# Kernel tuning notes

Hardware: AMD Instinct MI355X
Metric: run time of the kernel (lower is better)

Reference implementation:

```python
import jax, jax.numpy as jnp
import numpy as np

K_NB = 20  # num_neighbors

def _gather_nb(vals, idx):
    # vals: (B,N,D), idx: (B,N,K) -> (B,N,K,D)
    return jax.vmap(lambda v, i: v[i])(vals, idx)

def _pt_layer(x, pos, qkv_w, pw1, pb1, pw2, pb2, aw1, ab1, aw2, ab2):
    # x: (B,N,C), pos: (B,N,3)
    qkv = x @ qkv_w                      # (B,N,3C)
    q, k, v = jnp.split(qkv, 3, axis=-1)
    # squared euclidean distances (monotone in cdist -> same knn indices)
    d2 = jnp.sum((pos[:, :, None, :] - pos[:, None, :, :]) ** 2, axis=-1)  # (B,N,N)
    _, idx = jax.lax.top_k(-d2, K_NB)    # (B,N,K) smallest distances (incl. self)
    p2 = _gather_nb(pos, idx)            # (B,N,K,3)
    rel_pos = pos[:, :, None, :] - p2
    rel_pos_emb = jax.nn.relu(rel_pos @ pw1 + pb1) @ pw2 + pb2  # (B,N,K,C)
    k_nb = _gather_nb(k, idx)            # (B,N,K,C)
    qk_rel = q[:, :, None, :] - k_nb
    v_nb = _gather_nb(v, idx) + rel_pos_emb
    inp = jnp.concatenate([qk_rel, rel_pos_emb], axis=-1)  # (B,N,K,2C)
    sim = jax.nn.relu(inp @ aw1 + ab1) @ aw2 + ab2          # (B,N,K,1)
    attn = jax.nn.softmax(sim, axis=-2)
    return jnp.sum(attn * v_nb, axis=2)  # (B,N,C)

def setup_inputs() -> dict:
    key = jax.random.key(0)
    ks = jax.random.split(key, 32)
    B, N = 2, 8192
    s = 0.05
    d = {}
    d['points'] = jax.random.uniform(ks[0], (B, N, 3), jnp.float32)
    d['conv_w'] = jax.random.normal(ks[1], (3, 64), jnp.float32) * s
    d['conv_b'] = jax.random.normal(ks[2], (64,), jnp.float32) * s
    i = 3
    for L in ('l1', 'l2'):
        d[L + '_qkv'] = jax.random.normal(ks[i], (64, 192), jnp.float32) * s; i += 1
        d[L + '_pw1'] = jax.random.normal(ks[i], (3, 64), jnp.float32) * s; i += 1
        d[L + '_pb1'] = jax.random.normal(ks[i], (64,), jnp.float32) * s; i += 1
        d[L + '_pw2'] = jax.random.normal(ks[i], (64, 64), jnp.float32) * s; i += 1
        d[L + '_pb2'] = jax.random.normal(ks[i], (64,), jnp.float32) * s; i += 1
        d[L + '_aw1'] = jax.random.normal(ks[i], (128, 256), jnp.float32) * s; i += 1
        d[L + '_ab1'] = jax.random.normal(ks[i], (256,), jnp.float32) * s; i += 1
        d[L + '_aw2'] = jax.random.normal(ks[i], (256, 1), jnp.float32) * s; i += 1
        d[L + '_ab2'] = jax.random.normal(ks[i], (1,), jnp.float32) * s; i += 1
    d['fc1_w'] = jax.random.normal(ks[i], (64, 32), jnp.float32) * s; i += 1
    d['fc1_b'] = jax.random.normal(ks[i], (32,), jnp.float32) * s; i += 1
    d['fc3_w'] = jax.random.normal(ks[i], (32, 3), jnp.float32) * s; i += 1
    d['fc3_b'] = jax.random.normal(ks[i], (3,), jnp.float32) * s
    return d

def reference(points, conv_w, conv_b,
              l1_qkv, l1_pw1, l1_pb1, l1_pw2, l1_pb2, l1_aw1, l1_ab1, l1_aw2, l1_ab2,
              l2_qkv, l2_pw1, l2_pb1, l2_pw2, l2_pb2, l2_aw1, l2_ab1, l2_aw2, l2_ab2,
              fc1_w, fc1_b, fc3_w, fc3_b):
    pos = points
    out = jax.nn.relu(points @ conv_w + conv_b)  # Conv1d(3,64,1) == pointwise linear
    out = _pt_layer(out, pos, l1_qkv, l1_pw1, l1_pb1, l1_pw2, l1_pb2, l1_aw1, l1_ab1, l1_aw2, l1_ab2)
    out = _pt_layer(out, pos, l2_qkv, l2_pw1, l2_pb1, l2_pw2, l2_pb2, l2_aw1, l2_ab1, l2_aw2, l2_ab2)
    out = jnp.max(out, axis=1)                    # global max-pool over N
    out = jax.nn.relu(out @ fc1_w + fc1_b)
    return out @ fc3_w + fc3_b                    # (B, num_classes)
```

## Files before the change

kernel.cpp:

```cpp
#include <hip/hip_runtime.h>
#include <cstdint>
#include <cstddef>

#define KNB 20
#define NPTS 8192
#define BATCH 2
#define TOTAL (BATCH * NPTS)

__global__ __launch_bounds__(256) void k_conv(const float* __restrict__ pts,
                                              const float* __restrict__ w,
                                              const float* __restrict__ b,
                                              float* __restrict__ x0,
                                              float* __restrict__ ptsT) {
  int gid = blockIdx.x * 256 + threadIdx.x;
  if (gid >= TOTAL * 64) return;
  int p = gid >> 6, c = gid & 63;
  float px = pts[p * 3 + 0], py = pts[p * 3 + 1], pz = pts[p * 3 + 2];
  float acc = b[c] + px * w[c] + py * w[64 + c] + pz * w[128 + c];
  x0[gid] = fmaxf(acc, 0.f);
  if (c < 3) {
    int bb = p >> 13, pp = p & (NPTS - 1);
    ptsT[((size_t)bb * 3 + c) * NPTS + pp] = pts[p * 3 + c];
  }
}

__global__ __launch_bounds__(256) void k_knn(const float* __restrict__ ptsT,
                                             const float* __restrict__ pts,
                                             int* __restrict__ idxbuf) {
  int tid = threadIdx.x;
  int wv = tid >> 6, lane = tid & 63;
  int q = blockIdx.x * 4 + wv;
  int bq = q >> 13;
  const float* px = ptsT + (size_t)bq * 3 * NPTS;
  const float* py = px + NPTS;
  const float* pz = py + NPTS;
  float qx = pts[q * 3 + 0], qy = pts[q * 3 + 1], qz = pts[q * 3 + 2];

  float dist[KNB];
  int id[KNB];
#pragma unroll
  for (int j = 0; j < KNB; j++) { dist[j] = 3.402823466e38f; id[j] = 0; }
  float tau = 3.402823466e38f;

#define INSERT(D2, CID)                                                      \
  if ((D2) <= tau && (D2) < dist[KNB - 1]) {                                 \
    int cid_ = (CID);                                                        \
    _Pragma("unroll")                                                        \
    for (int j = KNB - 1; j >= 0; j--) {                                     \
      bool cj = (D2) < dist[j];                                              \
      bool cjm1 = (j > 0) && ((D2) < dist[j - 1]);                           \
      if (cj) {                                                              \
        dist[j] = cjm1 ? dist[j - 1] : (D2);                                 \
        id[j]   = cjm1 ? id[j - 1]   : cid_;                                 \
      }                                                                      \
    }                                                                        \
  }

  for (int chunk = 0; chunk < 8; chunk++) {
    if (chunk) {
      float h = dist[0];
#pragma unroll
      for (int k = 2; k <= 64; k <<= 1) {
#pragma unroll
        for (int j = k >> 1; j > 0; j >>= 1) {
          float o = __shfl_xor(h, j);
          bool up = ((lane & k) == 0);
          bool lower = ((lane & j) == 0);
          bool takeMin = (up == lower);
          bool lt = h < o;
          h = (takeMin == lt) ? h : o;
        }
      }
      tau = __shfl(h, 19);
    }

    int base = chunk * 1024;
#pragma unroll
    for (int g = 0; g < 4; g++) {
      int cb = base + g * 256 + lane * 4;
      float4 x4 = *(const float4*)&px[cb];
      float4 y4 = *(const float4*)&py[cb];
      float4 z4 = *(const float4*)&pz[cb];
      float dx0 = qx - x4.x, dy0 = qy - y4.x, dz0 = qz - z4.x;
      float dx1 = qx - x4.y, dy1 = qy - y4.y, dz1 = qz - z4.y;
      float dx2 = qx - x4.z, dy2 = qy - y4.z, dz2 = qz - z4.z;
      float dx3 = qx - x4.w, dy3 = qy - y4.w, dz3 = qz - z4.w;
      float d0 = __fadd_rn(__fadd_rn(__fmul_rn(dx0, dx0), __fmul_rn(dy0, dy0)),
                           __fmul_rn(dz0, dz0));
      float d1 = __fadd_rn(__fadd_rn(__fmul_rn(dx1, dx1), __fmul_rn(dy1, dy1)),
                           __fmul_rn(dz1, dz1));
      float d2v = __fadd_rn(__fadd_rn(__fmul_rn(dx2, dx2), __fmul_rn(dy2, dy2)),
                            __fmul_rn(dz2, dz2));
      float d3 = __fadd_rn(__fadd_rn(__fmul_rn(dx3, dx3), __fmul_rn(dy3, dy3)),
                           __fmul_rn(dz3, dz3));
      INSERT(d0, cb + 0)
      INSERT(d1, cb + 1)
      INSERT(d2v, cb + 2)
      INSERT(d3, cb + 3)
    }
  }
#undef INSERT

  int bqoff = bq * NPTS;
  for (int step = 0; step < KNB; step++) {
    unsigned long long p =
        ((unsigned long long)__float_as_uint(dist[0]) << 32) | (unsigned)id[0];
    unsigned long long m = p;
#pragma unroll
    for (int off = 32; off >= 1; off >>= 1) {
      unsigned long long o = __shfl_xor(m, off);
      m = (o < m) ? o : m;
    }
    if (lane == 0) idxbuf[q * KNB + step] = bqoff + (int)(m & 0xffffffffULL);
    if (p == m) {
#pragma unroll
      for (int j = 0; j < KNB - 1; j++) { dist[j] = dist[j + 1]; id[j] = id[j + 1]; }
      dist[KNB - 1] = 3.402823466e38f;
    }
  }
}

__global__ __launch_bounds__(256) void k_w2(const float* __restrict__ pw2,
                                            const float* __restrict__ pb2,
                                            const float* __restrict__ aw1,
                                            float* __restrict__ W2,
                                            float* __restrict__ c0) {
  int h = blockIdx.x, c = threadIdx.x;
  float a = 0.f;
  if (h < 64) {
#pragma unroll 8
    for (int j = 0; j < 64; j++)
      a += pw2[h * 64 + j] * aw1[(size_t)(64 + j) * 256 + c];
    W2[h * 256 + c] = a;
  } else {
#pragma unroll 8
    for (int j = 0; j < 64; j++)
      a += pb2[j] * aw1[(size_t)(64 + j) * 256 + c];
    c0[c] = a;
  }
}

__global__ __launch_bounds__(256) void k_pre(const float* __restrict__ x,
                                             const float* __restrict__ w,
                                             const float* __restrict__ aw1,
                                             const float* __restrict__ c0,
                                             float* __restrict__ v,
                                             float* __restrict__ kh,
                                             float* __restrict__ qh) {
  int tid = threadIdx.x;
  int wv = tid >> 6, lane = tid & 63;
  int p = blockIdx.x * 4 + wv;
  const float* xr = x + (size_t)p * 64;

  float qa = 0.f, ka = 0.f, va = 0.f;
#pragma unroll 8
  for (int h = 0; h < 64; h++) {
    float xv = xr[h];
    qa += xv * w[h * 192 + lane];
    ka += xv * w[h * 192 + 64 + lane];
    va += xv * w[h * 192 + 128 + lane];
  }
  v[(size_t)p * 64 + lane] = va;

#define RL(x_, l_) __uint_as_float(__builtin_amdgcn_readlane(__float_as_uint(x_), (l_)))
  int c4 = lane * 4;
  float4 a = make_float4(0.f, 0.f, 0.f, 0.f);
#pragma unroll 8
  for (int h = 0; h < 64; h++) {
    float kb = RL(ka, h);
    float4 wv4 = *(const float4*)&aw1[(size_t)h * 256 + c4];
    a.x += kb * wv4.x; a.y += kb * wv4.y; a.z += kb * wv4.z; a.w += kb * wv4.w;
  }
  *(float4*)&kh[(size_t)p * 256 + c4] = a;

  float4 b = make_float4(0.f, 0.f, 0.f, 0.f);
#pragma unroll 8
  for (int h = 0; h < 64; h++) {
    float qb = RL(qa, h);
    float4 wv4 = *(const float4*)&aw1[(size_t)h * 256 + c4];
    b.x += qb * wv4.x; b.y += qb * wv4.y; b.z += qb * wv4.z; b.w += qb * wv4.w;
  }
#undef RL
  float4 c04 = *(const float4*)&c0[c4];
  b.x += c04.x; b.y += c04.y; b.z += c04.z; b.w += c04.w;
  *(float4*)&qh[(size_t)p * 256 + c4] = b;
}

__global__ __launch_bounds__(256) void k_attn(
    const float* __restrict__ pos, const float* __restrict__ v,
    const int* __restrict__ idxbuf, const float* __restrict__ kh,
    const float* __restrict__ qh,
    const float* __restrict__ pw1, const float* __restrict__ pb1,
    const float* __restrict__ pw2, const float* __restrict__ pb2,
    const float* __restrict__ W2, const float* __restrict__ ab1,
    const float* __restrict__ aw2, const float* __restrict__ ab2,
    float* __restrict__ xout) {
  __shared__ float s_t1[4][KNB][64];
  __shared__ float s_sim[4][KNB];
  __shared__ int   s_nb[4][24];

  int tid = threadIdx.x;
  int wv = tid >> 6, lane = tid & 63;
  int i = blockIdx.x * 4 + wv;

  if (lane < KNB) s_nb[wv][lane] = idxbuf[i * KNB + lane];
  float px = pos[i * 3 + 0], py = pos[i * 3 + 1], pz = pos[i * 3 + 2];
  __syncthreads();

#define RL(x, l) __uint_as_float(__builtin_amdgcn_readlane(__float_as_uint(x), (l)))
  float t1[KNB];
  float vnb[KNB];
  {
    float w1x = pw1[lane], w1y = pw1[64 + lane], w1z = pw1[128 + lane];
    float b1h = pb1[lane];
#pragma unroll
    for (int n = 0; n < KNB; n++) {
      int g = s_nb[wv][n];
      vnb[n] = v[(size_t)g * 64 + lane];
      float rx = px - pos[g * 3 + 0];
      float ry = py - pos[g * 3 + 1];
      float rz = pz - pos[g * 3 + 2];
      t1[n] = fmaxf(b1h + rx * w1x + ry * w1y + rz * w1z, 0.f);
      s_t1[wv][n][lane] = t1[n];
    }
  }
  __syncthreads();

  int col0 = lane * 4;
  float4 qh4 = *(const float4*)&qh[(size_t)i * 256 + col0];

  float4 b1v = *(const float4*)&ab1[col0];
  float4 w2v = *(const float4*)&aw2[col0];
  float ab2v = ab2[0];
#pragma unroll
  for (int pass = 0; pass < 4; pass++) {
    int nb0 = pass * 5;
    float acc[5][4];
#pragma unroll
    for (int n = 0; n < 5; n++) {
      int g = s_nb[wv][nb0 + n];
      float4 kv = *(const float4*)&kh[(size_t)g * 256 + col0];
      acc[n][0] = qh4.x - kv.x; acc[n][1] = qh4.y - kv.y;
      acc[n][2] = qh4.z - kv.z; acc[n][3] = qh4.w - kv.w;
    }
#pragma unroll 2
    for (int kc = 0; kc < 64; kc += 4) {
      float4 w0 = *(const float4*)&W2[(kc + 0) * 256 + col0];
      float4 w1 = *(const float4*)&W2[(kc + 1) * 256 + col0];
      float4 w2 = *(const float4*)&W2[(kc + 2) * 256 + col0];
      float4 w3 = *(const float4*)&W2[(kc + 3) * 256 + col0];
#pragma unroll
      for (int n = 0; n < 5; n++) {
        float4 iv = *(float4*)&s_t1[wv][nb0 + n][kc];
        acc[n][0] += iv.x * w0.x + iv.y * w1.x + iv.z * w2.x + iv.w * w3.x;
        acc[n][1] += iv.x * w0.y + iv.y * w1.y + iv.z * w2.y + iv.w * w3.y;
        acc[n][2] += iv.x * w0.z + iv.y * w1.z + iv.z * w2.z + iv.w * w3.z;
        acc[n][3] += iv.x * w0.w + iv.y * w1.w + iv.z * w2.w + iv.w * w3.w;
      }
    }
#pragma unroll
    for (int n = 0; n < 5; n++) {
      float s = fmaxf(acc[n][0] + b1v.x, 0.f) * w2v.x +
                fmaxf(acc[n][1] + b1v.y, 0.f) * w2v.y +
                fmaxf(acc[n][2] + b1v.z, 0.f) * w2v.z +
                fmaxf(acc[n][3] + b1v.w, 0.f) * w2v.w;
#pragma unroll
      for (int off = 32; off >= 1; off >>= 1) s += __shfl_xor(s, off);
      if (lane == 0) s_sim[wv][nb0 + n] = s + ab2v;
    }
  }
  __syncthreads();

  float mx = -3.402823466e38f;
#pragma unroll
  for (int n = 0; n < KNB; n++) mx = fmaxf(mx, s_sim[wv][n]);
  float sum = 0.f;
#pragma unroll
  for (int n = 0; n < KNB; n++) sum += expf(s_sim[wv][n] - mx);
  float inv = 1.f / sum;
  float o = 0.f;
  float sac = 0.f;
#pragma unroll
  for (int n = 0; n < KNB; n++) {
    float an = expf(s_sim[wv][n] - mx) * inv;
    o += an * vnb[n];
    sac += an * t1[n];
  }
  float r = pb2[lane];
#pragma unroll 8
  for (int j = 0; j < 64; j++) r += RL(sac, j) * pw2[j * 64 + lane];
#undef RL
  xout[(size_t)i * 64 + lane] = o + r;
}

__global__ __launch_bounds__(256) void k_pool(const float* __restrict__ x,
                                              float* __restrict__ pmax) {
  __shared__ float red[4][64];
  int b = blockIdx.x >> 6, blk = blockIdx.x & 63;
  int tid = threadIdx.x;
  int c = tid & 63, pg = tid >> 6;
  int p0 = blk * 128;
  float mx = -3.402823466e38f;
  for (int p = pg; p < 128; p += 4)
    mx = fmaxf(mx, x[((size_t)b * NPTS + p0 + p) * 64 + c]);
  red[pg][c] = mx;
  __syncthreads();
  if (tid < 64)
    pmax[(size_t)blockIdx.x * 64 + c] =
        fmaxf(fmaxf(red[0][c], red[1][c]), fmaxf(red[2][c], red[3][c]));
}

__global__ __launch_bounds__(256) void k_final2(const float* __restrict__ pmax,
                                                const float* __restrict__ fc1w,
                                                const float* __restrict__ fc1b,
                                                const float* __restrict__ fc3w,
                                                const float* __restrict__ fc3b,
                                                float* __restrict__ out) {
  __shared__ float red[4][64];
  __shared__ float m[64];
  __shared__ float h1[32];
  int b = blockIdx.x;
  int tid = threadIdx.x;
  int c = tid & 63, pg = tid >> 6;
  float mx = -3.402823466e38f;
  for (int blk = pg; blk < 64; blk += 4)
    mx = fmaxf(mx, pmax[(size_t)(b * 64 + blk) * 64 + c]);
  red[pg][c] = mx;
  __syncthreads();
  if (tid < 64)
    m[c] = fmaxf(fmaxf(red[0][c], red[1][c]), fmaxf(red[2][c], red[3][c]));
  __syncthreads();
  if (tid < 32) {
    float a = fc1b[tid];
#pragma unroll 8
    for (int k = 0; k < 64; k++) a += m[k] * fc1w[k * 32 + tid];
    h1[tid] = fmaxf(a, 0.f);
  }
  __syncthreads();
  if (tid < 3) {
    float a = fc3b[tid];
#pragma unroll
    for (int k = 0; k < 32; k++) a += h1[k] * fc3w[k * 3 + tid];
    out[b * 3 + tid] = a;
  }
}

extern "C" void kernel_launch(void* const* d_in, const int* in_sizes, int n_in,
                              void* d_out, int out_size, void* d_ws,
                              size_t ws_size, hipStream_t stream) {
  const float* pts    = (const float*)d_in[0];
  const float* conv_w = (const float*)d_in[1];
  const float* conv_b = (const float*)d_in[2];
  const float* fc1w = (const float*)d_in[21];
  const float* fc1b = (const float*)d_in[22];
  const float* fc3w = (const float*)d_in[23];
  const float* fc3b = (const float*)d_in[24];
  float* outp = (float*)d_out;

  char* ws = (char*)d_ws;
  int*   idx  = (int*)  (ws);
  float* ptsT = (float*)(ws + (size_t)1536 * 1024);
  float* W2   = (float*)(ws + (size_t)1792 * 1024);
  float* c0   = (float*)(ws + (size_t)1862 * 1024);
  float* pmax = (float*)(ws + (size_t)1900 * 1024);
  float* v    = (float*)(ws + (size_t)2 * 1048576);
  float* kh   = (float*)(ws + (size_t)6656 * 1024);
  float* qh   = (float*)(ws + (size_t)24064 * 1024);
  float* act  = (float*)(ws + (size_t)41472 * 1024);

  k_conv<<<(TOTAL * 64 + 255) / 256, 256, 0, stream>>>(pts, conv_w, conv_b,
                                                       act, ptsT);
  k_knn<<<TOTAL / 4, 256, 0, stream>>>(ptsT, pts, idx);

  for (int layer = 0; layer < 2; layer++) {
    int base = 3 + layer * 9;
    const float* qkvw = (const float*)d_in[base + 0];
    const float* pw1  = (const float*)d_in[base + 1];
    const float* pb1  = (const float*)d_in[base + 2];
    const float* pw2  = (const float*)d_in[base + 3];
    const float* pb2  = (const float*)d_in[base + 4];
    const float* aw1  = (const float*)d_in[base + 5];
    const float* ab1  = (const float*)d_in[base + 6];
    const float* aw2  = (const float*)d_in[base + 7];
    const float* ab2  = (const float*)d_in[base + 8];
    k_w2<<<65, 256, 0, stream>>>(pw2, pb2, aw1, W2, c0);
    k_pre<<<TOTAL / 4, 256, 0, stream>>>(act, qkvw, aw1, c0, v, kh, qh);
    k_attn<<<TOTAL / 4, 256, 0, stream>>>(
        pts, v, idx, kh, qh, pw1, pb1, pw2, pb2, W2, ab1, aw2, ab2, act);
  }
  k_pool<<<BATCH * 64, 256, 0, stream>>>(act, pmax);
  k_final2<<<BATCH, 256, 0, stream>>>(pmax, fc1w, fc1b, fc3w, fc3b, outp);
}
```

Baseline: 1.027 ms.

## Replace brute-force kNN with uniform-grid spatial binning and local search

Points are binned into a 16^3 uniform grid per batch using histogram, scan and scatter kernels. Each query then searches only a 7x7x7 cell neighbourhood, and falls back to a full brute-force scan pruned by the 20th-smallest distance when that radius cannot guarantee exactness. This replaces the O(N^2) distance scan with mostly local work, at the cost of four extra small launches and divergent per-lane loops over cell ranges. Keys pack distance and original index into 64 bits so tie-breaking stays by index.

```diff
diff --git a/kernel.cpp b/kernel.cpp
--- a/kernel.cpp
+++ b/kernel.cpp
@@ -6,105 +6,178 @@
 #define NPTS 8192
 #define BATCH 2
 #define TOTAL (BATCH * NPTS)
+#define NCELL 4096
+#define SENT 0x7F800000FFFFFFFFULL
 
 __global__ __launch_bounds__(256) void k_conv(const float* __restrict__ pts,
                                               const float* __restrict__ w,
                                               const float* __restrict__ b,
-                                              float* __restrict__ x0,
-                                              float* __restrict__ ptsT) {
+                                              float* __restrict__ x0) {
   int gid = blockIdx.x * 256 + threadIdx.x;
   if (gid >= TOTAL * 64) return;
   int p = gid >> 6, c = gid & 63;
   float px = pts[p * 3 + 0], py = pts[p * 3 + 1], pz = pts[p * 3 + 2];
   float acc = b[c] + px * w[c] + py * w[64 + c] + pz * w[128 + c];
   x0[gid] = fmaxf(acc, 0.f);
-  if (c < 3) {
-    int bb = p >> 13, pp = p & (NPTS - 1);
-    ptsT[((size_t)bb * 3 + c) * NPTS + pp] = pts[p * 3 + c];
-  }
-}
-
-__global__ __launch_bounds__(256) void k_knn(const float* __restrict__ ptsT,
-                                             const float* __restrict__ pts,
-                                             int* __restrict__ idxbuf) {
+}
+
+__global__ __launch_bounds__(256) void k_zero(int* __restrict__ cnt) {
+  int g = blockIdx.x * 256 + threadIdx.x;
+  if (g < 2 * BATCH * NCELL) cnt[g] = 0;
+}
+
+__global__ __launch_bounds__(256) void k_hist(const float* __restrict__ pts,
+                                              int* __restrict__ cnt) {
+  int p = blockIdx.x * 256 + threadIdx.x;
+  if (p >= TOTAL) return;
+  int b = p >> 13;
+  int cx = min(15, (int)(pts[p * 3 + 0] * 16.f));
+  int cy = min(15, (int)(pts[p * 3 + 1] * 16.f));
+  int cz = min(15, (int)(pts[p * 3 + 2] * 16.f));
+  atomicAdd(&cnt[b * NCELL + (cz * 16 + cy) * 16 + cx], 1);
+}
+
+__global__ __launch_bounds__(256) void k_scan(const int* __restrict__ cnt,
+                                              int* __restrict__ cellStart) {
+  __shared__ int ls[256];
+  int b = blockIdx.x, t = threadIdx.x;
+  const int* c = cnt + b * NCELL;
+  int* cs = cellStart + b * (NCELL + 1);
+  int base = t * 16;
+  int s = 0;
+#pragma unroll
+  for (int i = 0; i < 16; i++) s += c[base + i];
+  ls[t] = s;
+  __syncthreads();
+  for (int off = 1; off < 256; off <<= 1) {
+    int v = (t >= off) ? ls[t - off] : 0;
+    __syncthreads();
+    ls[t] += v;
+    __syncthreads();
+  }
+  int run = ls[t] - s;
+#pragma unroll
+  for (int i = 0; i < 16; i++) { cs[base + i] = run; run += c[base + i]; }
+  if (t == 255) cs[NCELL] = run;
+}
+
+__global__ __launch_bounds__(256) void k_scatter(
+    const float* __restrict__ pts, int* __restrict__ cnt2,
+    const int* __restrict__ cellStart, float* __restrict__ sx,
+    float* __restrict__ sy, float* __restrict__ sz, int* __restrict__ sidx) {
+  int p = blockIdx.x * 256 + threadIdx.x;
+  if (p >= TOTAL) return;
+  int b = p >> 13, pl = p & (NPTS - 1);
+  float x = pts[p * 3 + 0], y = pts[p * 3 + 1], z = pts[p * 3 + 2];
+  int cx = min(15, (int)(x * 16.f));
+  int cy = min(15, (int)(y * 16.f));
+  int cz = min(15, (int)(z * 16.f));
+  int cell = (cz * 16 + cy) * 16 + cx;
+  int pos = cellStart[b * (NCELL + 1) + cell] + atomicAdd(&cnt2[b * NCELL + cell], 1);
+  size_t o = (size_t)b * NPTS + pos;
+  sx[o] = x; sy[o] = y; sz[o] = z; sidx[o] = pl;
+}
+
+__global__ __launch_bounds__(256) void k_knn(
+    const float* __restrict__ pts, const float* __restrict__ sx,
+    const float* __restrict__ sy, const float* __restrict__ sz,
+    const int* __restrict__ sidx, const int* __restrict__ cellStart,
+    int* __restrict__ idxbuf) {
   int tid = threadIdx.x;
   int wv = tid >> 6, lane = tid & 63;
   int q = blockIdx.x * 4 + wv;
   int bq = q >> 13;
-  const float* px = ptsT + (size_t)bq * 3 * NPTS;
-  const float* py = px + NPTS;
-  const float* pz = py + NPTS;
+  const float* bx = sx + (size_t)bq * NPTS;
+  const float* by = sy + (size_t)bq * NPTS;
+  const float* bz = sz + (size_t)bq * NPTS;
+  const int* bid = sidx + (size_t)bq * NPTS;
+  const int* cs = cellStart + bq * (NCELL + 1);
   float qx = pts[q * 3 + 0], qy = pts[q * 3 + 1], qz = pts[q * 3 + 2];
-
-  float dist[KNB];
-  int id[KNB];
-#pragma unroll
-  for (int j = 0; j < KNB; j++) { dist[j] = 3.402823466e38f; id[j] = 0; }
-  float tau = 3.402823466e38f;
-
-#define INSERT(D2, CID)                                                      \
-  if ((D2) <= tau && (D2) < dist[KNB - 1]) {                                 \
-    int cid_ = (CID);                                                        \
+  int cx = min(15, (int)(qx * 16.f));
+  int cy = min(15, (int)(qy * 16.f));
+  int cz = min(15, (int)(qz * 16.f));
+
+  unsigned long long key[KNB];
+#pragma unroll
+  for (int j = 0; j < KNB; j++) key[j] = SENT;
+
+#define INS(KK)                                                              \
+  if ((KK) < key[KNB - 1]) {                                                 \
     _Pragma("unroll")                                                        \
     for (int j = KNB - 1; j >= 0; j--) {                                     \
-      bool cj = (D2) < dist[j];                                              \
-      bool cjm1 = (j > 0) && ((D2) < dist[j - 1]);                           \
-      if (cj) {                                                              \
-        dist[j] = cjm1 ? dist[j - 1] : (D2);                                 \
-        id[j]   = cjm1 ? id[j - 1]   : cid_;                                 \
-      }                                                                      \
+      bool cj = (KK) < key[j];                                               \
+      bool cjm1 = (j > 0) && ((KK) < key[j - 1]);                            \
+      if (cj) key[j] = cjm1 ? key[j - 1] : (KK);                             \
     }                                                                        \
   }
 
-  for (int chunk = 0; chunk < 8; chunk++) {
-    if (chunk) {
-      float h = dist[0];
-#pragma unroll
-      for (int k = 2; k <= 64; k <<= 1) {
-#pragma unroll
-        for (int j = k >> 1; j > 0; j >>= 1) {
-          float o = __shfl_xor(h, j);
-          bool up = ((lane & k) == 0);
-          bool lower = ((lane & j) == 0);
-          bool takeMin = (up == lower);
-          bool lt = h < o;
-          h = (takeMin == lt) ? h : o;
-        }
+  if (lane < 49) {
+    int dz = lane / 7 - 3, dy = lane % 7 - 3;
+    int z = cz + dz, y = cy + dy;
+    if (z >= 0 && z < 16 && y >= 0 && y < 16) {
+      int x0 = cx - 3; if (x0 < 0) x0 = 0;
+      int x1 = cx + 3; if (x1 > 15) x1 = 15;
+      int rb = (z * 16 + y) * 16;
+      int s = cs[rb + x0], e = cs[rb + x1 + 1];
+      for (int i = s; i < e; i++) {
+        float dxv = qx - bx[i], dyv = qy - by[i], dzv = qz - bz[i];
+        float d2 = __fadd_rn(__fadd_rn(__fmul_rn(dxv, dxv), __fmul_rn(dyv, dyv)),
+                             __fmul_rn(dzv, dzv));
+        unsigned long long kk =
+            ((unsigned long long)__float_as_uint(d2) << 32) | (unsigned)bid[i];
+        INS(kk)
       }
-      tau = __shfl(h, 19);
-    }
-
-    int base = chunk * 1024;
-#pragma unroll
-    for (int g = 0; g < 4; g++) {
-      int cb = base + g * 256 + lane * 4;
-      float4 x4 = *(const float4*)&px[cb];
-      float4 y4 = *(const float4*)&py[cb];
-      float4 z4 = *(const float4*)&pz[cb];
-      float dx0 = qx - x4.x, dy0 = qy - y4.x, dz0 = qz - z4.x;
-      float dx1 = qx - x4.y, dy1 = qy - y4.y, dz1 = qz - z4.y;
-      float dx2 = qx - x4.z, dy2 = qy - y4.z, dz2 = qz - z4.z;
-      float dx3 = qx - x4.w, dy3 = qy - y4.w, dz3 = qz - z4.w;
-      float d0 = __fadd_rn(__fadd_rn(__fmul_rn(dx0, dx0), __fmul_rn(dy0, dy0)),
-                           __fmul_rn(dz0, dz0));
-      float d1 = __fadd_rn(__fadd_rn(__fmul_rn(dx1, dx1), __fmul_rn(dy1, dy1)),
-                           __fmul_rn(dz1, dz1));
-      float d2v = __fadd_rn(__fadd_rn(__fmul_rn(dx2, dx2), __fmul_rn(dy2, dy2)),
-                            __fmul_rn(dz2, dz2));
-      float d3 = __fadd_rn(__fadd_rn(__fmul_rn(dx3, dx3), __fmul_rn(dy3, dy3)),
-                           __fmul_rn(dz3, dz3));
-      INSERT(d0, cb + 0)
-      INSERT(d1, cb + 1)
-      INSERT(d2v, cb + 2)
-      INSERT(d3, cb + 3)
-    }
-  }
-#undef INSERT
+    }
+  }
+
+  float h = __uint_as_float((unsigned)(key[0] >> 32));
+#pragma unroll
+  for (int k = 2; k <= 64; k <<= 1) {
+#pragma unroll
+    for (int j = k >> 1; j > 0; j >>= 1) {
+      float o = __shfl_xor(h, j);
+      bool up = ((lane & k) == 0);
+      bool lower = ((lane & j) == 0);
+      bool takeMin = (up == lower);
+      bool lt = h < o;
+      h = (takeMin == lt) ? h : o;
+    }
+  }
+  float tau19 = __shfl(h, 19);
+
+  if (!(tau19 < 0.0351f)) {
+#pragma unroll
+    for (int j = 0; j < KNB; j++) key[j] = SENT;
+    for (int g = 0; g < 32; g++) {
+      int i0 = g * 256 + lane * 4;
+      float4 x4 = *(const float4*)&bx[i0];
+      float4 y4 = *(const float4*)&by[i0];
+      float4 z4 = *(const float4*)&bz[i0];
+#define FB(C, XX, YY, ZZ)                                                    \
+      {                                                                      \
+        float dxv = qx - (XX), dyv = qy - (YY), dzv = qz - (ZZ);             \
+        float d2 = __fadd_rn(__fadd_rn(__fmul_rn(dxv, dxv),                  \
+                                       __fmul_rn(dyv, dyv)),                 \
+                             __fmul_rn(dzv, dzv));                           \
+        if (d2 <= tau19) {                                                   \
+          unsigned long long kk =                                            \
+              ((unsigned long long)__float_as_uint(d2) << 32) |              \
+              (unsigned)bid[i0 + (C)];                                       \
+          INS(kk)                                                            \
+        }                                                                    \
+      }
+      FB(0, x4.x, y4.x, z4.x)
+      FB(1, x4.y, y4.y, z4.y)
+      FB(2, x4.z, y4.z, z4.z)
+      FB(3, x4.w, y4.w, z4.w)
+#undef FB
+    }
+  }
+#undef INS
 
   int bqoff = bq * NPTS;
   for (int step = 0; step < KNB; step++) {
-    unsigned long long p =
-        ((unsigned long long)__float_as_uint(dist[0]) << 32) | (unsigned)id[0];
+    unsigned long long p = key[0];
     unsigned long long m = p;
 #pragma unroll
     for (int off = 32; off >= 1; off >>= 1) {
@@ -114,8 +187,8 @@
     if (lane == 0) idxbuf[q * KNB + step] = bqoff + (int)(m & 0xffffffffULL);
     if (p == m) {
 #pragma unroll
-      for (int j = 0; j < KNB - 1; j++) { dist[j] = dist[j + 1]; id[j] = id[j + 1]; }
-      dist[KNB - 1] = 3.402823466e38f;
+      for (int j = 0; j < KNB - 1; j++) key[j] = key[j + 1];
+      key[KNB - 1] = SENT;
     }
   }
 }
@@ -358,19 +431,29 @@
   float* outp = (float*)d_out;
 
   char* ws = (char*)d_ws;
-  int*   idx  = (int*)  (ws);
-  float* ptsT = (float*)(ws + (size_t)1536 * 1024);
-  float* W2   = (float*)(ws + (size_t)1792 * 1024);
-  float* c0   = (float*)(ws + (size_t)1862 * 1024);
-  float* pmax = (float*)(ws + (size_t)1900 * 1024);
-  float* v    = (float*)(ws + (size_t)2 * 1048576);
-  float* kh   = (float*)(ws + (size_t)6656 * 1024);
-  float* qh   = (float*)(ws + (size_t)24064 * 1024);
-  float* act  = (float*)(ws + (size_t)41472 * 1024);
-
-  k_conv<<<(TOTAL * 64 + 255) / 256, 256, 0, stream>>>(pts, conv_w, conv_b,
-                                                       act, ptsT);
-  k_knn<<<TOTAL / 4, 256, 0, stream>>>(ptsT, pts, idx);
+  int*   idx   = (int*)  (ws);
+  float* sx    = (float*)(ws + (size_t)1408 * 1024);
+  float* sy    = (float*)(ws + (size_t)1472 * 1024);
+  float* sz    = (float*)(ws + (size_t)1536 * 1024);
+  int*   sidx  = (int*)  (ws + (size_t)1600 * 1024);
+  float* W2    = (float*)(ws + (size_t)1664 * 1024);
+  float* c0    = (float*)(ws + (size_t)1728 * 1024);
+  float* pmax  = (float*)(ws + (size_t)1732 * 1024);
+  int*   cellS = (int*)  (ws + (size_t)1764 * 1024);
+  int*   cnt   = (int*)  (ws + (size_t)1800 * 1024);
+  int*   cnt2  = cnt + BATCH * NCELL;
+  float* v     = (float*)(ws + (size_t)2 * 1048576);
+  float* kh    = (float*)(ws + (size_t)6656 * 1024);
+  float* qh    = (float*)(ws + (size_t)24064 * 1024);
+  float* act   = (float*)(ws + (size_t)41472 * 1024);
+
+  k_conv<<<(TOTAL * 64 + 255) / 256, 256, 0, stream>>>(pts, conv_w, conv_b, act);
+  k_zero<<<(2 * BATCH * NCELL + 255) / 256, 256, 0, stream>>>(cnt);
+  k_hist<<<(TOTAL + 255) / 256, 256, 0, stream>>>(pts, cnt);
+  k_scan<<<BATCH, 256, 0, stream>>>(cnt, cellS);
+  k_scatter<<<(TOTAL + 255) / 256, 256, 0, stream>>>(pts, cnt2, cellS, sx, sy,
+                                                     sz, sidx);
+  k_knn<<<TOTAL / 4, 256, 0, stream>>>(pts, sx, sy, sz, sidx, cellS, idx);
 
   for (int layer = 0; layer < 2; layer++) {
     int base = 3 + layer * 9;
```

New measurement: 1.006 ms. 2.1% less time.
